# Performance work log

Hardware: AMD Instinct MI355X
Metric: run time of the kernel (lower is better)

Reference implementation:

```python
import jax, jax.numpy as jnp
from jax import lax
import numpy as np

EPS = 1e-5


def ref_points(Hk, Wk):
    # torch linspace(0.5, Hk-0.5, Hk)/Hk * 2 - 1, stacked (y, x)
    ys = (jnp.linspace(0.5, Hk - 0.5, Hk) / Hk) * 2.0 - 1.0
    xs = (jnp.linspace(0.5, Wk - 0.5, Wk) / Wk) * 2.0 - 1.0
    yy, xx = jnp.meshgrid(ys, xs, indexing='ij')
    return jnp.stack([yy, xx], axis=-1)  # (Hk, Wk, 2) in (y, x) order


def grid_sample(img, grid):
    # Bilinear, align_corners=True, zeros padding (torch F.grid_sample defaults).
    # img: (N, C, Hi, Wi); grid: (N, Hg, Wg, 2) with (x, y) in [-1, 1].
    N, C, Hi, Wi = img.shape
    Hg, Wg = grid.shape[1], grid.shape[2]
    gx = (grid[..., 0] + 1.0) * 0.5 * (Wi - 1)
    gy = (grid[..., 1] + 1.0) * 0.5 * (Hi - 1)
    x0 = jnp.floor(gx)
    y0 = jnp.floor(gy)
    wx1 = gx - x0
    wy1 = gy - y0
    imgf = img.reshape(N, C, Hi * Wi)

    def corner(ix, iy, w):
        valid = (ix >= 0) & (ix < Wi) & (iy >= 0) & (iy < Hi)
        idx = (jnp.clip(iy, 0, Hi - 1).astype(jnp.int32) * Wi
               + jnp.clip(ix, 0, Wi - 1).astype(jnp.int32)).reshape(N, -1)
        vals = jax.vmap(lambda im, f: im[:, f])(imgf, idx)  # (N, C, Hg*Wg)
        return vals * (w * valid).reshape(N, 1, -1)

    out = (corner(x0, y0, (1 - wx1) * (1 - wy1))
           + corner(x0 + 1, y0, wx1 * (1 - wy1))
           + corner(x0, y0 + 1, (1 - wx1) * wy1)
           + corner(x0 + 1, y0 + 1, wx1 * wy1))
    return out.reshape(N, C, Hg, Wg)


def setup_inputs() -> dict:
    key = jax.random.key(0)
    ks = jax.random.split(key, 8)
    B, C, H, W = 8, 128, 64, 64
    gc, nH = 64, 4
    return {
        'x': jax.random.normal(ks[0], (B, C, H, W), jnp.float32),
        'w_dw': jax.random.normal(ks[1], (gc, 1, 5, 5), jnp.float32) * 0.1,
        'ln_w': jnp.ones((gc,), jnp.float32),
        'w_off': jax.random.normal(ks[2], (3, gc), jnp.float32) * 0.1,
        'wq': jax.random.normal(ks[3], (C, C), jnp.float32) * 0.05,
        'wk': jax.random.normal(ks[4], (C, C), jnp.float32) * 0.05,
        'wv': jax.random.normal(ks[5], (C, C), jnp.float32) * 0.05,
        'wo': jax.random.normal(ks[6], (C, C), jnp.float32) * 0.05,
        'rpe': jax.random.normal(ks[7], (nH, 2 * H - 1, 2 * W - 1), jnp.float32) * 0.01,
    }


def reference(x, w_dw, ln_w, w_off, wq, wk, wv, wo, rpe):
    B, C, H, W = x.shape
    G, nH = 2, 4
    gc = C // G           # group channels
    dh = C // nH          # head channels
    gh = nH // G          # heads per group
    scale = dh ** -0.5
    orf = 1.0             # offset_range_factor

    conv1x1 = lambda t, w: jnp.einsum('oi,bihw->bohw', w, t)

    q = conv1x1(x, wq)                                    # (B, C, H, W)
    q_off = q.reshape(B * G, gc, H, W)

    # conv_offset: depthwise 5x5 stride 4 pad 2 -> BiasFree LN (over C) -> GELU -> 1x1 to 3
    off = lax.conv_general_dilated(q_off, w_dw, (4, 4), ((2, 2), (2, 2)),
                                   dimension_numbers=('NCHW', 'OIHW', 'NCHW'),
                                   feature_group_count=gc)  # (B*G, gc, Hk, Wk)
    var = jnp.var(off, axis=1, keepdims=True)
    off = off / jnp.sqrt(var + EPS) * ln_w.reshape(1, -1, 1, 1)
    off = jax.nn.gelu(off, approximate=False)
    off = jnp.einsum('oi,bihw->bohw', w_off, off)          # (B*G, 3, Hk, Wk)

    Hk, Wk = off.shape[2], off.shape[3]
    n = Hk * Wk

    # channel 0 = y offset, channel 1 = x offset, channel 2 = modulation
    offset = jnp.stack([jnp.tanh(off[:, 0]) * (orf / Hk),
                        jnp.tanh(off[:, 1]) * (orf / Wk)], axis=-1)  # (B*G, Hk, Wk, 2) (y,x)
    dm = jax.nn.sigmoid(off[:, 2])[:, None]                # (B*G, 1, Hk, Wk)

    pos = offset + ref_points(Hk, Wk)[None]                # (B*G, Hk, Wk, 2) (y,x)

    xs = grid_sample(x.reshape(B * G, gc, H, W), pos[..., ::-1])  # grid in (x,y)
    xs = (xs * dm).reshape(B, C, 1, n)

    k = conv1x1(xs, wk).reshape(B * nH, dh, n)
    v = conv1x1(xs, wv).reshape(B * nH, dh, n)
    qf = q.reshape(B * nH, dh, H * W)

    attn = jnp.einsum('bcm,bcn->bmn', qf, k) * scale       # (B*nH, H*W, n)

    # relative-position bias sampled at continuous displacements
    rpe_b = jnp.broadcast_to(rpe[None], (B, nH, 2 * H - 1, 2 * W - 1)
                             ).reshape(B * G, gh, 2 * H - 1, 2 * W - 1)
    qg = ref_points(H, W).reshape(H * W, 2)                # (H*W, 2)
    disp = (qg[None, :, None, :] - pos.reshape(B * G, 1, n, 2)) * 0.5  # (B*G, H*W, n, 2)
    bias = grid_sample(rpe_b, disp[..., ::-1]).reshape(B * nH, H * W, n)

    attn = jax.nn.softmax(attn + bias, axis=2)
    out = jnp.einsum('bmn,bcn->bcm', attn, v).reshape(B, C, H, W)
    return conv1x1(out, wo)
```

## Files before the change

### kernel.cpp

```cpp
#include <hip/hip_runtime.h>
#include <hip/hip_bf16.h>
#include <math.h>

#define HW 4096
#define NCH 128

typedef __attribute__((ext_vector_type(8))) short short8;
typedef __attribute__((ext_vector_type(4))) float f32x4;

__device__ __forceinline__ short f2bf(float f) {
  union { __hip_bfloat16 h; short s; } u;
  u.h = __float2bfloat16(f);
  return u.s;
}
__device__ __forceinline__ float bf2f(short s) {
  union { unsigned u; float f; } u;
  u.u = ((unsigned)(unsigned short)s) << 16;
  return u.f;
}
__device__ __forceinline__ float upk(unsigned u) {
  union { unsigned u; float f; } a, b;
  a.u = u & 0xFFFF0000u;
  b.u = u << 16;
  return a.f + b.f;
}

__global__ __launch_bounds__(256) void xq_kernel(
    const float* __restrict__ x, const float* __restrict__ wq,
    unsigned* __restrict__ xpk, float* __restrict__ qT) {
  __shared__ float s[128][65];
  int tid = threadIdx.x;
  int b = blockIdx.y;
  int m0 = blockIdx.x * 64;
  {
    int ml = tid & 63, ch = tid >> 6;
#pragma unroll
    for (int i = 0; i < 32; ++i) {
      int c = i * 4 + ch;
      s[c][ml] = x[((size_t)(b * NCH + c)) * HW + m0 + ml];
    }
  }
  __syncthreads();
  {
    int c = tid & 127, mh = tid >> 7;
#pragma unroll
    for (int i = 0; i < 32; ++i) {
      int m = i * 2 + mh;
      float v = s[c][m];
      short hi = f2bf(v);
      unsigned lo = (unsigned short)f2bf(v - bf2f(hi));
      xpk[((size_t)(b * HW + m0 + m)) * NCH + c] =
          (((unsigned)(unsigned short)hi) << 16) | lo;
    }
  }
  int w = tid >> 6, lane = tid & 63, l15 = lane & 15, qd = lane >> 4;
  int mrow = w * 16 + l15;
  f32x4 acc[8];
#pragma unroll
  for (int ot = 0; ot < 8; ++ot) acc[ot] = (f32x4){0.f, 0.f, 0.f, 0.f};
#pragma unroll
  for (int kc = 0; kc < 4; ++kc) {
    short8 ah, al;
#pragma unroll
    for (int j = 0; j < 8; ++j) {
      float v = s[kc * 32 + qd * 8 + j][mrow];
      short hi = f2bf(v);
      ah[j] = hi;
      al[j] = f2bf(v - bf2f(hi));
    }
#pragma unroll
    for (int ot = 0; ot < 8; ++ot) {
      const float* wr = wq + (size_t)(ot * 16 + l15) * NCH + kc * 32 + qd * 8;
      f32x4 w0 = *(const f32x4*)wr;
      f32x4 w1 = *(const f32x4*)(wr + 4);
      short8 bh, bl;
#pragma unroll
      for (int j = 0; j < 4; ++j) {
        short h0 = f2bf(w0[j]);
        bh[j] = h0;
        bl[j] = f2bf(w0[j] - bf2f(h0));
        short h1 = f2bf(w1[j]);
        bh[4 + j] = h1;
        bl[4 + j] = f2bf(w1[j] - bf2f(h1));
      }
      acc[ot] = __builtin_amdgcn_mfma_f32_16x16x32_bf16(ah, bh, acc[ot], 0, 0, 0);
      acc[ot] = __builtin_amdgcn_mfma_f32_16x16x32_bf16(al, bh, acc[ot], 0, 0, 0);
      acc[ot] = __builtin_amdgcn_mfma_f32_16x16x32_bf16(ah, bl, acc[ot], 0, 0, 0);
    }
  }
#pragma unroll
  for (int ot = 0; ot < 8; ++ot)
#pragma unroll
    for (int r = 0; r < 4; ++r)
      qT[((size_t)(b * HW + m0 + w * 16 + qd * 4 + r)) * NCH + ot * 16 + l15] =
          acc[ot][r];
}

__device__ __forceinline__ float wsum64(float v) {
#pragma unroll
  for (int o = 32; o > 0; o >>= 1) v += __shfl_xor(v, o);
  return v;
}

__global__ __launch_bounds__(256) void offs_kernel(
    const float* __restrict__ qT, const float* __restrict__ w_dw,
    const float* __restrict__ ln_w, const float* __restrict__ w_off,
    const unsigned* __restrict__ xpk, const float* __restrict__ wk,
    const float* __restrict__ wv, const float* __restrict__ wo,
    const float* __restrict__ rpe, float* __restrict__ pos,
    short* __restrict__ xsT, short* __restrict__ wk_bf,
    short* __restrict__ wv_bf, short* __restrict__ wo_bf,
    _Float16* __restrict__ rpe16) {
  int tid = threadIdx.x;
  int bid = blockIdx.x;
  if (bid >= 256) {
    if (bid < 320) {
      int i = (bid - 256) * 256 + tid;
      wk_bf[i] = f2bf(wk[i]);
      wv_bf[i] = f2bf(wv[i]);
      wo_bf[i] = f2bf(wo[i]);
    } else {
      int i = (bid - 320) * 256 + tid;
      if (i < 4 * 16800) {
        int h = i / 16800, r = i % 16800;
        int y = r / 130, xx = r % 130;
        float v = 0.f;
        if (y >= 1 && y <= 127 && xx >= 1 && xx <= 127)
          v = rpe[(size_t)h * 16129 + (y - 1) * 127 + (xx - 1)];
        rpe16[i] = (_Float16)v;
      }
    }
    return;
  }
  int bg = bid >> 4;
  int p0 = (bid & 15) * 16;
  int c = tid & 63;
  int w = tid >> 6;
  int b = bg >> 1, ch0 = (bg & 1) * 64;
  const float* qp = qT + (size_t)b * HW * NCH + ch0 + c;
  const float* wd = w_dw + c * 25;
  float pyr[4], pxr[4], dmr[4];
#pragma unroll
  for (int i = 0; i < 4; ++i) {
    int p = p0 + w * 4 + i;
    int py = p >> 4, px = p & 15;
    float acc = 0.f;
#pragma unroll
    for (int ky = 0; ky < 5; ++ky) {
      int iy = 4 * py + ky - 2;
      if (iy < 0 || iy >= 64) continue;
#pragma unroll
      for (int kx = 0; kx < 5; ++kx) {
        int ix = 4 * px + kx - 2;
        if (ix < 0 || ix >= 64) continue;
        acc += wd[ky * 5 + kx] * qp[(size_t)(iy * 64 + ix) * NCH];
      }
    }
    float mean = wsum64(acc) * (1.f / 64.f);
    float msq = wsum64(acc * acc) * (1.f / 64.f);
    float var = msq - mean * mean;
    float g = acc * rsqrtf(var + 1e-5f) * ln_w[c];
    g = 0.5f * g * (1.f + erff(g * 0.70710678118654752f));
    float o0 = wsum64(w_off[c] * g);
    float o1 = wsum64(w_off[64 + c] * g);
    float o2 = wsum64(w_off[128 + c] * g);
    pyr[i] = tanhf(o0) * (1.f / 16.f) + ((py + 0.5f) * (1.f / 8.f) - 1.f);
    pxr[i] = tanhf(o1) * (1.f / 16.f) + ((px + 0.5f) * (1.f / 8.f) - 1.f);
    dmr[i] = 1.f / (1.f + expf(-o2));
    if (c == 0) {
      int idx = bg * 256 + p;
      pos[idx * 2] = pyr[i];
      pos[idx * 2 + 1] = pxr[i];
    }
  }
  size_t rb = (size_t)b * HW * NCH + ch0 + c;
#pragma unroll
  for (int i = 0; i < 4; ++i) {
    int p = p0 + w * 4 + i;
    float gx = (pxr[i] + 1.f) * 31.5f;
    float gy = (pyr[i] + 1.f) * 31.5f;
    float x0f = floorf(gx), y0f = floorf(gy);
    int ix = (int)x0f, iy = (int)y0f;
    float fx = gx - x0f, fy = gy - y0f;
    float w00 = (1.f - fx) * (1.f - fy), w10 = fx * (1.f - fy);
    float w01 = (1.f - fx) * fy, w11 = fx * fy;
    bool vx0 = (ix >= 0 && ix < 64), vx1 = (ix + 1 >= 0 && ix + 1 < 64);
    bool vy0 = (iy >= 0 && iy < 64), vy1 = (iy + 1 >= 0 && iy + 1 < 64);
    if (!(vx0 && vy0)) w00 = 0.f;
    if (!(vx1 && vy0)) w10 = 0.f;
    if (!(vx0 && vy1)) w01 = 0.f;
    if (!(vx1 && vy1)) w11 = 0.f;
    int x0c = min(max(ix, 0), 63), x1c = min(max(ix + 1, 0), 63);
    int y0c = min(max(iy, 0), 63), y1c = min(max(iy + 1, 0), 63);
    float v = w00 * upk(xpk[rb + (size_t)(y0c * 64 + x0c) * NCH]) +
              w10 * upk(xpk[rb + (size_t)(y0c * 64 + x1c) * NCH]) +
              w01 * upk(xpk[rb + (size_t)(y1c * 64 + x0c) * NCH]) +
              w11 * upk(xpk[rb + (size_t)(y1c * 64 + x1c) * NCH]);
    xsT[((size_t)(b * 256 + p)) * NCH + ch0 + c] = f2bf(v * dmr[i]);
  }
}

__global__ __launch_bounds__(256) void kv_mfma_kernel(
    const short* __restrict__ xsT, const short* __restrict__ wk_bf,
    const short* __restrict__ wv_bf, short* __restrict__ kbf,
    short* __restrict__ vbf) {
  int tid = threadIdx.x;
  int w = tid >> 6, lane = tid & 63, l15 = lane & 15, qd = lane >> 4;
  int bh = blockIdx.x, b = bh >> 2;
  int n0 = blockIdx.y * 64 + w * 16;
  f32x4 acc[2];
  acc[0] = (f32x4){0.f, 0.f, 0.f, 0.f};
  acc[1] = (f32x4){0.f, 0.f, 0.f, 0.f};

  size_t xrow = ((size_t)(b * 256 + n0 + l15)) * NCH + qd * 8;
  if (blockIdx.z == 0) {
#pragma unroll
    for (int kc = 0; kc < 4; ++kc) {
      short8 a = *(const short8*)&xsT[xrow + kc * 32];
#pragma unroll
      for (int ot = 0; ot < 2; ++ot) {
        short8 bb = *(const short8*)&wk_bf[(size_t)((bh & 3) * 32 + ot * 16 + l15) * NCH + kc * 32 + qd * 8];
        acc[ot] = __builtin_amdgcn_mfma_f32_16x16x32_bf16(a, bb, acc[ot], 0, 0, 0);
      }
    }
#pragma unroll
    for (int ot = 0; ot < 2; ++ot)
#pragma unroll
      for (int r = 0; r < 4; ++r)
        kbf[((size_t)(bh * 256 + n0 + qd * 4 + r)) * 32 + ot * 16 + l15] =
            f2bf(acc[ot][r]);
  } else {
#pragma unroll
    for (int kc = 0; kc < 4; ++kc) {
      short8 bb = *(const short8*)&xsT[xrow + kc * 32];
#pragma unroll
      for (int ot = 0; ot < 2; ++ot) {
        short8 a = *(const short8*)&wv_bf[(size_t)((bh & 3) * 32 + ot * 16 + l15) * NCH + kc * 32 + qd * 8];
        acc[ot] = __builtin_amdgcn_mfma_f32_16x16x32_bf16(a, bb, acc[ot], 0, 0, 0);
      }
    }
#pragma unroll
    for (int ot = 0; ot < 2; ++ot)
#pragma unroll
      for (int r = 0; r < 4; ++r)
        vbf[((size_t)(bh * 32 + ot * 16 + qd * 4 + r)) * 256 + n0 + l15] =
            f2bf(acc[ot][r]);
  }
}

#define PROW 264
#define POS_OFF 33552
#define LDS_BYTES 35600

__global__ __launch_bounds__(256) void attn_kernel(
    const float* __restrict__ qT, const short* __restrict__ kbf,
    const short* __restrict__ vbf, const float* __restrict__ pos,
    const _Float16* __restrict__ rpe16, short* __restrict__ outT) {
  __shared__ __align__(16) unsigned char s_raw[LDS_BYTES];
  _Float16* tab = (_Float16*)s_raw;
  float* s_pos = (float*)(s_raw + POS_OFF);
  short* s_p = (short*)s_raw;

  int tid = threadIdx.x;
  int wv = tid >> 6;
  int lane = tid & 63;
  int l15 = lane & 15;
  int qd = lane >> 4;
  int bh = blockIdx.y;
  int b = bh >> 2, h = bh & 3;
  int bg = b * 2 + (h >> 1);
  int m0 = blockIdx.x * 64 + wv * 16;

  {
    const uint4* src = (const uint4*)(rpe16 + (size_t)h * 16800);
    uint4* dst = (uint4*)s_raw;
    for (int i = tid; i < 2097; i += 256) dst[i] = src[i];
    const float* posg = pos + (size_t)bg * 512;
    s_pos[tid] = posg[tid];
    s_pos[256 + tid] = posg[256 + tid];
  }

  short8 qfrag;
  {
    const float* qg = qT + ((size_t)(b * HW + m0 + l15)) * NCH + h * 32 + qd * 8;
    f32x4 a0 = *(const f32x4*)qg;
    f32x4 a1 = *(const f32x4*)(qg + 4);
#pragma unroll
    for (int j = 0; j < 4; ++j) {
      qfrag[j] = f2bf(a0[j]);
      qfrag[4 + j] = f2bf(a1[j]);
    }
  }

  f32x4 acc[16];
  {
    const short* kb = kbf + ((size_t)bh * 256 + l15) * 32 + qd * 8;
#pragma unroll
    for (int t = 0; t < 16; ++t) {
      short8 kf = *(const short8*)(kb + t * 16 * 32);
      acc[t] = __builtin_amdgcn_mfma_f32_16x16x32_bf16(
          kf, qfrag, (f32x4){0.f, 0.f, 0.f, 0.f}, 0, 0, 0);
    }
  }
  __syncthreads();

  int m = m0 + l15;
  float gy0 = ((((float)(m >> 6) + 0.5f) * (1.f / 32.f) - 1.f) * 0.5f + 1.f) * 63.f;
  float gx0 = ((((float)(m & 63) + 0.5f) * (1.f / 32.f) - 1.f) * 0.5f + 1.f) * 63.f;
  float mx = -1e30f;
#pragma unroll
  for (int t = 0; t < 16; ++t) {
    const f32x4* pp4 = (const f32x4*)&s_pos[(t * 16 + qd * 4) * 2];
    f32x4 pA = pp4[0];
    f32x4 pB = pp4[1];
    float py[4] = {pA[0], pA[2], pB[0], pB[2]};
    float px[4] = {pA[1], pA[3], pB[1], pB[3]};
#pragma unroll
    for (int r = 0; r < 4; ++r) {
      float gy = gy0 - py[r] * 31.5f;
      float gx = gx0 - px[r] * 31.5f;
      float y0f = floorf(gy), x0f = floorf(gx);
      float fy = gy - y0f, fx = gx - x0f;
      int base = (int)y0f * 130 + (int)x0f + 131;
      unsigned u0, u1;
      __builtin_memcpy(&u0, (const char*)tab + 2 * base, 4);
      __builtin_memcpy(&u1, (const char*)tab + 2 * base + 260, 4);
      union { unsigned u; _Float16 h[2]; } c0, c1;
      c0.u = u0;
      c1.u = u1;
      float t00 = (float)c0.h[0], t10 = (float)c0.h[1];
      float t01 = (float)c1.h[0], t11 = (float)c1.h[1];
      float r0 = t00 + fx * (t10 - t00);
      float r1 = t01 + fx * (t11 - t01);
      float bias = r0 + fy * (r1 - r0);
      float s = fmaf(acc[t][r], 0.17677669529663688f, bias);
      acc[t][r] = s;
      mx = fmaxf(mx, s);
    }
  }
  mx = fmaxf(mx, __shfl_xor(mx, 16));
  float M = fmaxf(mx, __shfl_xor(mx, 32));

  float sm = 0.f;
#pragma unroll
  for (int t = 0; t < 16; ++t) {
#pragma unroll
    for (int r = 0; r < 4; ++r) {
      float e = __expf(acc[t][r] - M);
      acc[t][r] = e;
      sm += e;
    }
  }
  sm += __shfl_xor(sm, 16);
  sm += __shfl_xor(sm, 32);
  float inv = 1.f / sm;

  __syncthreads();

  {
    short* pw = s_p + wv * 16 * PROW + l15 * PROW;
#pragma unroll
    for (int t = 0; t < 16; ++t) {
      int n = t * 16 + qd * 4;
      short4 pk;
      pk.x = f2bf(acc[t][0]);
      pk.y = f2bf(acc[t][1]);
      pk.z = f2bf(acc[t][2]);
      pk.w = f2bf(acc[t][3]);
      *(short4*)(pw + n) = pk;
    }
  }

  f32x4 o0 = {0.f, 0.f, 0.f, 0.f}, o1 = {0.f, 0.f, 0.f, 0.f};
  {
    const short* vb = vbf + ((size_t)bh * 32 + l15) * 256 + qd * 8;
    const short* pr = s_p + wv * 16 * PROW + l15 * PROW + qd * 8;
#pragma unroll
    for (int ch = 0; ch < 8; ++ch) {
      short8 pf = *(const short8*)(pr + ch * 32);
      short8 v0 = *(const short8*)(vb + ch * 32);
      short8 v1 = *(const short8*)(vb + 16 * 256 + ch * 32);
      o0 = __builtin_amdgcn_mfma_f32_16x16x32_bf16(v0, pf, o0, 0, 0, 0);
      o1 = __builtin_amdgcn_mfma_f32_16x16x32_bf16(v1, pf, o1, 0, 0, 0);
    }
  }
  {
    size_t row = (size_t)(b * HW + m0 + l15) * NCH + h * 32 + qd * 4;
    short4 s0, s1;
    s0.x = f2bf(o0[0] * inv); s0.y = f2bf(o0[1] * inv);
    s0.z = f2bf(o0[2] * inv); s0.w = f2bf(o0[3] * inv);
    s1.x = f2bf(o1[0] * inv); s1.y = f2bf(o1[1] * inv);
    s1.z = f2bf(o1[2] * inv); s1.w = f2bf(o1[3] * inv);
    *(short4*)&outT[row] = s0;
    *(short4*)&outT[row + 16] = s1;
  }
}

__global__ __launch_bounds__(256) void wo_mfma_kernel(
    const short* __restrict__ attnT, const short* __restrict__ wo_bf,
    float* __restrict__ out) {
  int tid = threadIdx.x;
  int wv = tid >> 6;
  int lane = tid & 63;
  int l15 = lane & 15;
  int qd = lane >> 4;
  int b = blockIdx.x >> 6;
  int m0 = (blockIdx.x & 63) * 64 + wv * 16;

  f32x4 acc[8];
#pragma unroll
  for (int ot = 0; ot < 8; ++ot) acc[ot] = (f32x4){0.f, 0.f, 0.f, 0.f};

  const short* arow = attnT + (size_t)(b * HW + m0 + l15) * NCH + qd * 8;
  const short* wrow = wo_bf + (size_t)l15 * NCH + qd * 8;
#pragma unroll
  for (int kc = 0; kc < 4; ++kc) {
    short8 afrag = *(const short8*)(arow + kc * 32);
#pragma unroll
    for (int ot = 0; ot < 8; ++ot) {
      short8 bfrag = *(const short8*)(wrow + (size_t)ot * 16 * NCH + kc * 32);
      acc[ot] = __builtin_amdgcn_mfma_f32_16x16x32_bf16(afrag, bfrag, acc[ot],
                                                        0, 0, 0);
    }
  }
#pragma unroll
  for (int ot = 0; ot < 8; ++ot) {
    float* op = out + ((size_t)b * NCH + ot * 16 + l15) * HW + m0 + qd * 4;
    *(f32x4*)op = acc[ot];
  }
}

extern "C" void kernel_launch(void* const* d_in, const int* in_sizes, int n_in,
                              void* d_out, int out_size, void* d_ws,
                              size_t ws_size, hipStream_t stream) {
  const float* x = (const float*)d_in[0];
  const float* w_dw = (const float*)d_in[1];
  const float* ln_w = (const float*)d_in[2];
  const float* w_off = (const float*)d_in[3];
  const float* wq = (const float*)d_in[4];
  const float* wk = (const float*)d_in[5];
  const float* wv = (const float*)d_in[6];
  const float* wo = (const float*)d_in[7];
  const float* rpe = (const float*)d_in[8];
  float* out = (float*)d_out;

  float* qT = out;
  short* sb = (short*)d_ws;
  unsigned* xpk = (unsigned*)sb;
  short* outT = sb;
  short* xsT = sb + 8388608;
  short* kbf = sb + 8650752;
  short* vbf = sb + 8912896;
  short* wk_bf = sb + 9175040;
  short* wv_bf = sb + 9191424;
  short* wo_bf = sb + 9207808;
  _Float16* rpe16 = (_Float16*)(sb + 9224192);
  float* pos = (float*)(sb + 9291392);

  xq_kernel<<<dim3(64, 8), 256, 0, stream>>>(x, wq, xpk, qT);
  offs_kernel<<<583, 256, 0, stream>>>(qT, w_dw, ln_w, w_off, xpk, wk, wv, wo,
                                       rpe, pos, xsT, wk_bf, wv_bf, wo_bf,
                                       rpe16);
  kv_mfma_kernel<<<dim3(32, 4, 2), 256, 0, stream>>>(xsT, wk_bf, wv_bf, kbf,
                                                     vbf);
  attn_kernel<<<dim3(64, 32), 256, 0, stream>>>(qT, kbf, vbf, pos, rpe16,
                                                outT);
  wo_mfma_kernel<<<512, 256, 0, stream>>>(outT, wo_bf, out);
}
```

Baseline: 189.5 us.

## Split offset kernel, store x as single bf16, repack RPE table row-paired

The x transpose now stores one bf16 per element instead of a packed hi/lo pair, which halves that buffer and lowers sampled-x precision. The offset kernel is split into a conv/offset kernel with one point per wave and a separate bilinear sampling kernel, which adds a launch but gives more parallel blocks. The RPE bias table is repacked as 128-wide rows, each entry holding two fp16 values from vertically adjacent rows, so the attention kernel reads two aligned 32-bit LDS words per sample. Positions are now read from global memory instead of LDS.

```diff
diff --git a/kernel.cpp b/kernel.cpp
--- a/kernel.cpp
+++ b/kernel.cpp
@@ -18,16 +18,10 @@
   u.u = ((unsigned)(unsigned short)s) << 16;
   return u.f;
 }
-__device__ __forceinline__ float upk(unsigned u) {
-  union { unsigned u; float f; } a, b;
-  a.u = u & 0xFFFF0000u;
-  b.u = u << 16;
-  return a.f + b.f;
-}
 
 __global__ __launch_bounds__(256) void xq_kernel(
     const float* __restrict__ x, const float* __restrict__ wq,
-    unsigned* __restrict__ xpk, float* __restrict__ qT) {
+    short* __restrict__ xT, float* __restrict__ qT) {
   __shared__ float s[128][65];
   int tid = threadIdx.x;
   int b = blockIdx.y;
@@ -46,11 +40,7 @@
 #pragma unroll
     for (int i = 0; i < 32; ++i) {
       int m = i * 2 + mh;
-      float v = s[c][m];
-      short hi = f2bf(v);
-      unsigned lo = (unsigned short)f2bf(v - bf2f(hi));
-      xpk[((size_t)(b * HW + m0 + m)) * NCH + c] =
-          (((unsigned)(unsigned short)hi) << 16) | lo;
+      xT[((size_t)(b * HW + m0 + m)) * NCH + c] = f2bf(s[c][m]);
     }
   }
   int w = tid >> 6, lane = tid & 63, l15 = lane & 15, qd = lane >> 4;
@@ -102,102 +92,104 @@
   return v;
 }
 
-__global__ __launch_bounds__(256) void offs_kernel(
+__global__ __launch_bounds__(256) void conv_offset_kernel(
     const float* __restrict__ qT, const float* __restrict__ w_dw,
     const float* __restrict__ ln_w, const float* __restrict__ w_off,
-    const unsigned* __restrict__ xpk, const float* __restrict__ wk,
-    const float* __restrict__ wv, const float* __restrict__ wo,
-    const float* __restrict__ rpe, float* __restrict__ pos,
-    short* __restrict__ xsT, short* __restrict__ wk_bf,
-    short* __restrict__ wv_bf, short* __restrict__ wo_bf,
-    _Float16* __restrict__ rpe16) {
-  int tid = threadIdx.x;
-  int bid = blockIdx.x;
-  if (bid >= 256) {
-    if (bid < 320) {
-      int i = (bid - 256) * 256 + tid;
+    const float* __restrict__ wk, const float* __restrict__ wv,
+    const float* __restrict__ wo, const float* __restrict__ rpe,
+    float* __restrict__ pos, float* __restrict__ dm,
+    short* __restrict__ wk_bf, short* __restrict__ wv_bf,
+    short* __restrict__ wo_bf, unsigned* __restrict__ tab) {
+  int tid = threadIdx.x;
+  if (blockIdx.x >= 64) {
+    int id = (blockIdx.x - 64) * 16 + blockIdx.y;
+    if (id < 64) {
+      int i = id * 256 + tid;
       wk_bf[i] = f2bf(wk[i]);
       wv_bf[i] = f2bf(wv[i]);
       wo_bf[i] = f2bf(wo[i]);
     } else {
-      int i = (bid - 320) * 256 + tid;
-      if (i < 4 * 16800) {
-        int h = i / 16800, r = i % 16800;
-        int y = r / 130, xx = r % 130;
-        float v = 0.f;
-        if (y >= 1 && y <= 127 && xx >= 1 && xx <= 127)
-          v = rpe[(size_t)h * 16129 + (y - 1) * 127 + (xx - 1)];
-        rpe16[i] = (_Float16)v;
+      int i = (id - 64) * 256 + tid;
+      int h = i >> 14, r = i & 16383;
+      int row = r >> 7, col = r & 127;
+      float lo = 0.f, hi = 0.f;
+      if (col < 127) {
+        if (row >= 1) lo = rpe[h * 16129 + (row - 1) * 127 + col];
+        if (row < 127) hi = rpe[h * 16129 + row * 127 + col];
       }
+      union { unsigned u; _Float16 h2[2]; } pk;
+      pk.h2[0] = (_Float16)lo;
+      pk.h2[1] = (_Float16)hi;
+      tab[i] = pk.u;
     }
     return;
   }
-  int bg = bid >> 4;
-  int p0 = (bid & 15) * 16;
   int c = tid & 63;
-  int w = tid >> 6;
+  int p = blockIdx.x * 4 + (tid >> 6);
+  int bg = blockIdx.y;
+  int py = p >> 4, px = p & 15;
+  const float* qp = qT + (size_t)(bg >> 1) * HW * NCH + (bg & 1) * 64 + c;
+  const float* wd = w_dw + c * 25;
+  float acc = 0.f;
+#pragma unroll
+  for (int ky = 0; ky < 5; ++ky) {
+    int iy = 4 * py + ky - 2;
+    if (iy < 0 || iy >= 64) continue;
+#pragma unroll
+    for (int kx = 0; kx < 5; ++kx) {
+      int ix = 4 * px + kx - 2;
+      if (ix < 0 || ix >= 64) continue;
+      acc += wd[ky * 5 + kx] * qp[(size_t)(iy * 64 + ix) * NCH];
+    }
+  }
+  float mean = wsum64(acc) * (1.f / 64.f);
+  float msq = wsum64(acc * acc) * (1.f / 64.f);
+  float var = msq - mean * mean;
+  float g = acc * rsqrtf(var + 1e-5f) * ln_w[c];
+  g = 0.5f * g * (1.f + erff(g * 0.70710678118654752f));
+  float o0 = wsum64(w_off[c] * g);
+  float o1 = wsum64(w_off[64 + c] * g);
+  float o2 = wsum64(w_off[128 + c] * g);
+  if (c == 0) {
+    int idx = bg * 256 + p;
+    pos[idx * 2] = tanhf(o0) * (1.f / 16.f) + ((py + 0.5f) * (1.f / 8.f) - 1.f);
+    pos[idx * 2 + 1] = tanhf(o1) * (1.f / 16.f) + ((px + 0.5f) * (1.f / 8.f) - 1.f);
+    dm[idx] = 1.f / (1.f + expf(-o2));
+  }
+}
+
+__global__ __launch_bounds__(256) void sample_xs_kernel(
+    const short* __restrict__ xT, const float* __restrict__ pos,
+    const float* __restrict__ dm, short* __restrict__ xsT) {
+  int tid = threadIdx.x;
+  int c = tid & 63;
+  int p = blockIdx.y * 4 + (tid >> 6);
+  int bg = blockIdx.x;
   int b = bg >> 1, ch0 = (bg & 1) * 64;
-  const float* qp = qT + (size_t)b * HW * NCH + ch0 + c;
-  const float* wd = w_dw + c * 25;
-  float pyr[4], pxr[4], dmr[4];
-#pragma unroll
-  for (int i = 0; i < 4; ++i) {
-    int p = p0 + w * 4 + i;
-    int py = p >> 4, px = p & 15;
-    float acc = 0.f;
-#pragma unroll
-    for (int ky = 0; ky < 5; ++ky) {
-      int iy = 4 * py + ky - 2;
-      if (iy < 0 || iy >= 64) continue;
-#pragma unroll
-      for (int kx = 0; kx < 5; ++kx) {
-        int ix = 4 * px + kx - 2;
-        if (ix < 0 || ix >= 64) continue;
-        acc += wd[ky * 5 + kx] * qp[(size_t)(iy * 64 + ix) * NCH];
-      }
-    }
-    float mean = wsum64(acc) * (1.f / 64.f);
-    float msq = wsum64(acc * acc) * (1.f / 64.f);
-    float var = msq - mean * mean;
-    float g = acc * rsqrtf(var + 1e-5f) * ln_w[c];
-    g = 0.5f * g * (1.f + erff(g * 0.70710678118654752f));
-    float o0 = wsum64(w_off[c] * g);
-    float o1 = wsum64(w_off[64 + c] * g);
-    float o2 = wsum64(w_off[128 + c] * g);
-    pyr[i] = tanhf(o0) * (1.f / 16.f) + ((py + 0.5f) * (1.f / 8.f) - 1.f);
-    pxr[i] = tanhf(o1) * (1.f / 16.f) + ((px + 0.5f) * (1.f / 8.f) - 1.f);
-    dmr[i] = 1.f / (1.f + expf(-o2));
-    if (c == 0) {
-      int idx = bg * 256 + p;
-      pos[idx * 2] = pyr[i];
-      pos[idx * 2 + 1] = pxr[i];
-    }
-  }
+  int idx = bg * 256 + p;
+  float posy = pos[idx * 2], posx = pos[idx * 2 + 1];
+  float dmv = dm[idx];
+  float gx = (posx + 1.f) * 31.5f;
+  float gy = (posy + 1.f) * 31.5f;
+  float x0f = floorf(gx), y0f = floorf(gy);
+  int ix = (int)x0f, iy = (int)y0f;
+  float fx = gx - x0f, fy = gy - y0f;
+  float w00 = (1.f - fx) * (1.f - fy), w10 = fx * (1.f - fy);
+  float w01 = (1.f - fx) * fy, w11 = fx * fy;
+  bool vx0 = (ix >= 0 && ix < 64), vx1 = (ix + 1 >= 0 && ix + 1 < 64);
+  bool vy0 = (iy >= 0 && iy < 64), vy1 = (iy + 1 >= 0 && iy + 1 < 64);
+  if (!(vx0 && vy0)) w00 = 0.f;
+  if (!(vx1 && vy0)) w10 = 0.f;
+  if (!(vx0 && vy1)) w01 = 0.f;
+  if (!(vx1 && vy1)) w11 = 0.f;
+  int x0c = min(max(ix, 0), 63), x1c = min(max(ix + 1, 0), 63);
+  int y0c = min(max(iy, 0), 63), y1c = min(max(iy + 1, 0), 63);
   size_t rb = (size_t)b * HW * NCH + ch0 + c;
-#pragma unroll
-  for (int i = 0; i < 4; ++i) {
-    int p = p0 + w * 4 + i;
-    float gx = (pxr[i] + 1.f) * 31.5f;
-    float gy = (pyr[i] + 1.f) * 31.5f;
-    float x0f = floorf(gx), y0f = floorf(gy);
-    int ix = (int)x0f, iy = (int)y0f;
-    float fx = gx - x0f, fy = gy - y0f;
-    float w00 = (1.f - fx) * (1.f - fy), w10 = fx * (1.f - fy);
-    float w01 = (1.f - fx) * fy, w11 = fx * fy;
-    bool vx0 = (ix >= 0 && ix < 64), vx1 = (ix + 1 >= 0 && ix + 1 < 64);
-    bool vy0 = (iy >= 0 && iy < 64), vy1 = (iy + 1 >= 0 && iy + 1 < 64);
-    if (!(vx0 && vy0)) w00 = 0.f;
-    if (!(vx1 && vy0)) w10 = 0.f;
-    if (!(vx0 && vy1)) w01 = 0.f;
-    if (!(vx1 && vy1)) w11 = 0.f;
-    int x0c = min(max(ix, 0), 63), x1c = min(max(ix + 1, 0), 63);
-    int y0c = min(max(iy, 0), 63), y1c = min(max(iy + 1, 0), 63);
-    float v = w00 * upk(xpk[rb + (size_t)(y0c * 64 + x0c) * NCH]) +
-              w10 * upk(xpk[rb + (size_t)(y0c * 64 + x1c) * NCH]) +
-              w01 * upk(xpk[rb + (size_t)(y1c * 64 + x0c) * NCH]) +
-              w11 * upk(xpk[rb + (size_t)(y1c * 64 + x1c) * NCH]);
-    xsT[((size_t)(b * 256 + p)) * NCH + ch0 + c] = f2bf(v * dmr[i]);
-  }
+  float v = w00 * bf2f(xT[rb + (size_t)(y0c * 64 + x0c) * NCH]) +
+            w10 * bf2f(xT[rb + (size_t)(y0c * 64 + x1c) * NCH]) +
+            w01 * bf2f(xT[rb + (size_t)(y1c * 64 + x0c) * NCH]) +
+            w11 * bf2f(xT[rb + (size_t)(y1c * 64 + x1c) * NCH]);
+  xsT[((size_t)(b * 256 + p)) * NCH + ch0 + c] = f2bf(v * dmv);
 }
 
 __global__ __launch_bounds__(256) void kv_mfma_kernel(
@@ -249,17 +241,13 @@
 }
 
 #define PROW 264
-#define POS_OFF 33552
-#define LDS_BYTES 35600
 
 __global__ __launch_bounds__(256) void attn_kernel(
     const float* __restrict__ qT, const short* __restrict__ kbf,
     const short* __restrict__ vbf, const float* __restrict__ pos,
-    const _Float16* __restrict__ rpe16, short* __restrict__ outT) {
-  __shared__ __align__(16) unsigned char s_raw[LDS_BYTES];
-  _Float16* tab = (_Float16*)s_raw;
-  float* s_pos = (float*)(s_raw + POS_OFF);
-  short* s_p = (short*)s_raw;
+    const unsigned* __restrict__ tabg, short* __restrict__ outT) {
+  __shared__ __align__(16) unsigned s_tab[16384];
+  short* s_p = (short*)s_tab;
 
   int tid = threadIdx.x;
   int wv = tid >> 6;
@@ -272,12 +260,9 @@
   int m0 = blockIdx.x * 64 + wv * 16;
 
   {
-    const uint4* src = (const uint4*)(rpe16 + (size_t)h * 16800);
-    uint4* dst = (uint4*)s_raw;
-    for (int i = tid; i < 2097; i += 256) dst[i] = src[i];
-    const float* posg = pos + (size_t)bg * 512;
-    s_pos[tid] = posg[tid];
-    s_pos[256 + tid] = posg[256 + tid];
+    const uint4* src = (const uint4*)(tabg + (size_t)h * 16384);
+    uint4* dst = (uint4*)s_tab;
+    for (int i = tid; i < 4096; i += 256) dst[i] = src[i];
   }
 
   short8 qfrag;
@@ -307,10 +292,11 @@
   int m = m0 + l15;
   float gy0 = ((((float)(m >> 6) + 0.5f) * (1.f / 32.f) - 1.f) * 0.5f + 1.f) * 63.f;
   float gx0 = ((((float)(m & 63) + 0.5f) * (1.f / 32.f) - 1.f) * 0.5f + 1.f) * 63.f;
+  const float* posg = pos + (size_t)bg * 512;
   float mx = -1e30f;
 #pragma unroll
   for (int t = 0; t < 16; ++t) {
-    const f32x4* pp4 = (const f32x4*)&s_pos[(t * 16 + qd * 4) * 2];
+    const f32x4* pp4 = (const f32x4*)&posg[(t * 16 + qd * 4) * 2];
     f32x4 pA = pp4[0];
     f32x4 pB = pp4[1];
     float py[4] = {pA[0], pA[2], pB[0], pB[2]};
@@ -321,15 +307,15 @@
       float gx = gx0 - px[r] * 31.5f;
       float y0f = floorf(gy), x0f = floorf(gx);
       float fy = gy - y0f, fx = gx - x0f;
-      int base = (int)y0f * 130 + (int)x0f + 131;
-      unsigned u0, u1;
-      __builtin_memcpy(&u0, (const char*)tab + 2 * base, 4);
-      __builtin_memcpy(&u1, (const char*)tab + 2 * base + 260, 4);
-      union { unsigned u; _Float16 h[2]; } c0, c1;
-      c0.u = u0;
-      c1.u = u1;
-      float t00 = (float)c0.h[0], t10 = (float)c0.h[1];
-      float t01 = (float)c1.h[0], t11 = (float)c1.h[1];
+      int row = ((int)y0f + 1) << 7;
+      int xl = (int)x0f;
+      unsigned left = s_tab[row + (xl & 127)];
+      unsigned right = s_tab[row + xl + 1];
+      union { unsigned u; _Float16 h2[2]; } L, R;
+      L.u = left;
+      R.u = right;
+      float t00 = (float)L.h2[0], t01 = (float)L.h2[1];
+      float t10 = (float)R.h2[0], t11 = (float)R.h2[1];
       float r0 = t00 + fx * (t10 - t00);
       float r1 = t01 + fx * (t11 - t01);
       float bias = r0 + fy * (r1 - r0);
@@ -446,24 +432,25 @@
 
   float* qT = out;
   short* sb = (short*)d_ws;
-  unsigned* xpk = (unsigned*)sb;
+  short* xT = sb;
   short* outT = sb;
-  short* xsT = sb + 8388608;
-  short* kbf = sb + 8650752;
-  short* vbf = sb + 8912896;
-  short* wk_bf = sb + 9175040;
-  short* wv_bf = sb + 9191424;
-  short* wo_bf = sb + 9207808;
-  _Float16* rpe16 = (_Float16*)(sb + 9224192);
-  float* pos = (float*)(sb + 9291392);
-
-  xq_kernel<<<dim3(64, 8), 256, 0, stream>>>(x, wq, xpk, qT);
-  offs_kernel<<<583, 256, 0, stream>>>(qT, w_dw, ln_w, w_off, xpk, wk, wv, wo,
-                                       rpe, pos, xsT, wk_bf, wv_bf, wo_bf,
-                                       rpe16);
+  short* xsT = sb + 4194304;
+  short* kbf = sb + 4456448;
+  short* vbf = sb + 4718592;
+  short* wk_bf = sb + 4980736;
+  short* wv_bf = sb + 4997120;
+  short* wo_bf = sb + 5013504;
+  unsigned* tab = (unsigned*)(sb + 5029888);
+  float* pos = (float*)(sb + 5160960);
+  float* dm = pos + 8192;
+
+  xq_kernel<<<dim3(64, 8), 256, 0, stream>>>(x, wq, xT, qT);
+  conv_offset_kernel<<<dim3(84, 16), 256, 0, stream>>>(
+      qT, w_dw, ln_w, w_off, wk, wv, wo, rpe, pos, dm, wk_bf, wv_bf, wo_bf,
+      tab);
+  sample_xs_kernel<<<dim3(16, 64), 256, 0, stream>>>(xT, pos, dm, xsT);
   kv_mfma_kernel<<<dim3(32, 4, 2), 256, 0, stream>>>(xsT, wk_bf, wv_bf, kbf,
                                                      vbf);
-  attn_kernel<<<dim3(64, 32), 256, 0, stream>>>(qT, kbf, vbf, pos, rpe16,
-                                                outT);
+  attn_kernel<<<dim3(64, 32), 256, 0, stream>>>(qT, kbf, vbf, pos, tab, outT);
   wo_mfma_kernel<<<512, 256, 0, stream>>>(outT, wo_bf, out);
 }
```

Result: no change. 190.5 us (+0.5%).
